# Optimization experiments

Measured on AMD Instinct MI355X. Metric: run time of the kernel, lower is better.

The kernel has to match this reference:

```python
import jax, jax.numpy as jnp
import numpy as np

LOSS_WEIGHT = 1.0
EPS = 1e-12  # numerical floor under the sqrt (module's eps)


def setup_inputs() -> dict:
    key = jax.random.key(0)
    k1, k2 = jax.random.split(key)
    N, P1, P2, D = 16, 4096, 4096, 2
    point_set_1 = jax.random.normal(k1, (N, P1, D), dtype=jnp.float32)
    point_set_2 = jax.random.normal(k2, (N, P2, D), dtype=jnp.float32)
    return {"point_set_1": point_set_1, "point_set_2": point_set_2}


def _chamfer_per_object(x, y):
    # x: [N, P1, 2], y: [N, P2, 2]
    # Pairwise squared L2 via expansion |x|^2 + |y|^2 - 2<x,y> (avoids [N,P1,P2,2] diff tensor)
    x2 = jnp.sum(x * x, axis=-1)                       # [N, P1]
    y2 = jnp.sum(y * y, axis=-1)                       # [N, P2]
    xy = jnp.einsum('npd,nqd->npq', x, y)              # [N, P1, P2]
    C = jnp.sqrt(jnp.clip(x2[:, :, None] + y2[:, None, :] - 2.0 * xy, EPS))  # [N, P1, P2]
    d1 = jnp.min(C, axis=-1).mean(axis=-1)             # min over P2, mean over P1 -> [N]
    d2 = jnp.min(C, axis=-2).mean(axis=-1)             # min over P1, mean over P2 -> [N]
    return 0.5 * (d1 + d2)                             # [N]


def reference(point_set_1, point_set_2):
    # Vectorized form of the per-object Python loop:
    # each object's chamfer (reduction='mean' over a batch of 1 == identity)
    # is masked by (set_2.sum() >= 0), summed, and divided by n_obj.
    cost = _chamfer_per_object(point_set_1, point_set_2)                 # [N]
    m = (jnp.sum(point_set_2, axis=(-1, -2)) >= 0).astype(cost.dtype)    # [N]
    return jnp.mean(cost * m) * LOSS_WEIGHT                              # scalar
```

## Files before the change

kernel.cpp:

```cpp
#include <hip/hip_runtime.h>
#include <math.h>

#define N_OBJ 16
#define P 4096
#define BLOCK 256
#define EPSF 1e-12f

#define G 96
#define GG (G * G)
#define NGRID (2 * N_OBJ)
#define LO (-6.0f)
#define CELL 0.125f
#define INV_CELL 8.0f
#define BPT (GG / BLOCK)
#define QPB (BLOCK / 4)
#define QBLOCKS (2 * N_OBJ * P / QPB)


__device__ __forceinline__ float wave_sum(float s) {
#pragma unroll
    for (int off = 32; off > 0; off >>= 1)
        s += __shfl_xor(s, off, 64);
    return s;
}

__global__ __launch_bounds__(BLOCK) void k_build(const float* __restrict__ s1,
                                                 const float* __restrict__ s2,
                                                 float2* __restrict__ pts,
                                                 unsigned* __restrict__ binStart,
                                                 unsigned* __restrict__ maskws) {
    int gid = blockIdx.x;
    int n = gid >> 1, t = gid & 1;
    int tid = threadIdx.x;
    const float2* src = (const float2*)(t ? s1 : s2) + n * P;

    __shared__ unsigned cnt[GG];
    __shared__ unsigned wtot[BLOCK / 64];
    __shared__ float wq[BLOCK / 64];

    for (int i = tid; i < GG; i += BLOCK) cnt[i] = 0u;
    __syncthreads();

    float2 p[16];
    int b[16];
    float msum = 0.0f;
#pragma unroll
    for (int k = 0; k < 16; k++) {
        float2 v = src[k * BLOCK + tid];
        p[k] = v;
        msum += v.x + v.y;
        int bx = (int)((v.x - LO) * INV_CELL);
        int by = (int)((v.y - LO) * INV_CELL);
        bx = min(max(bx, 0), G - 1);
        by = min(max(by, 0), G - 1);
        b[k] = by * G + bx;
        atomicAdd(&cnt[b[k]], 1u);
    }
    msum = wave_sum(msum);
    if ((tid & 63) == 0) wq[tid >> 6] = msum;
    __syncthreads();
    if (t == 0 && tid == 0) {
        float total = (wq[0] + wq[1]) + (wq[2] + wq[3]);
        maskws[n] = (total >= 0.0f) ? 1u : 0u;
    }

    unsigned run = 0;
    int base = tid * BPT;
    for (int i = 0; i < BPT; i++) {
        unsigned cv = cnt[base + i];
        cnt[base + i] = run;
        run += cv;
    }
    unsigned x = run;
#pragma unroll
    for (int off = 1; off < 64; off <<= 1) {
        unsigned v = __shfl_up(x, off, 64);
        if ((tid & 63) >= off) x += v;
    }
    if ((tid & 63) == 63) wtot[tid >> 6] = x;
    __syncthreads();
    unsigned wpre = 0;
    for (int w2 = 0; w2 < (tid >> 6); w2++) wpre += wtot[w2];
    unsigned offs = wpre + x - run;
    for (int i = 0; i < BPT; i++) cnt[base + i] += offs;
    __syncthreads();

    unsigned* bs = binStart + (size_t)gid * (GG + 1);
    for (int i = tid; i < GG; i += BLOCK) bs[i] = cnt[i];
    if (tid == 0) bs[GG] = P;
    __syncthreads();

    float2* dst = pts + (size_t)gid * P;
#pragma unroll
    for (int k = 0; k < 16; k++) {
        unsigned idx = atomicAdd(&cnt[b[k]], 1u);
        dst[idx] = p[k];
    }
}

#define CAND_LOOP(ss, ee)                                   \
    for (unsigned i = (ss) + sub; i < (ee); i += 4) {       \
        float2 y = tp[i];                                   \
        float y2 = fmaf(y.x, y.x, y.y * y.y);               \
        float d  = fmaf(nqy, y.y, y2);                      \
        d = fmaf(nqx, y.x, d);                              \
        m = fminf(m, d);                                    \
    }

__global__ __launch_bounds__(BLOCK) void k_query(const float2* __restrict__ pts,
                                                 const unsigned* __restrict__ binStart,
                                                 const unsigned* __restrict__ maskws,
                                                 float* __restrict__ out) {
    int bid = blockIdx.x;
    int tid = threadIdx.x;
    int sub = tid & 3;
    int qi  = bid * QPB + (tid >> 2);
    int pass = qi >> 16;
    int n    = (qi >> 12) & 15;
    int qoff = qi & 4095;
    __shared__ float wq[BLOCK / 64];

    if (maskws[n] == 0u) return;

    int g_tgt = n * 2 + pass;
    int g_src = n * 2 + (1 - pass);
    const float2* tp   = pts + (size_t)g_tgt * P;
    const unsigned* bs = binStart + (size_t)g_tgt * (GG + 1);

    float2 q = pts[(size_t)g_src * P + qoff];
    float c   = fmaf(q.x, q.x, q.y * q.y);
    float nqx = -2.0f * q.x, nqy = -2.0f * q.y;
    int bx = min(max((int)((q.x - LO) * INV_CELL), 0), G - 1);
    int by = min(max((int)((q.y - LO) * INV_CELL), 0), G - 1);

    float m = INFINITY;

    for (int dy = 0; dy < G; dy++) {
        if (dy >= 2) {
            float bb = (float)(dy - 1) * CELL;
            if (bb * bb > m + c) break;
        }
        float mc = fmaxf(m + c, 0.0f);
        float sr = sqrtf(mc);
        int w = (sr >= 11.9f) ? G : (int)(sr * INV_CELL) + 2;
        int xs = max(bx - w, 0), xe = min(bx + w, G - 1);

        int yU = by + dy, yD = by - dy;
        unsigned sU = 0u, eU = 0u, sD = 0u, eD = 0u;
        if (yU <= G - 1)          { sU = bs[yU * G + xs]; eU = bs[yU * G + xe + 1]; }
        if (dy > 0 && yD >= 0)    { sD = bs[yD * G + xs]; eD = bs[yD * G + xe + 1]; }
        CAND_LOOP(sU, eU)
        CAND_LOOP(sD, eD)

        m = fminf(m, __shfl_xor(m, 1, 64));
        m = fminf(m, __shfl_xor(m, 2, 64));
    }

    float dq = (sub == 0) ? sqrtf(fmaxf(m + c, EPSF)) : 0.0f;
    dq = wave_sum(dq);
    if ((tid & 63) == 0) wq[tid >> 6] = dq;
    __syncthreads();
    if (tid == 0) {
        float sum = (wq[0] + wq[1]) + (wq[2] + wq[3]);
        atomicAdd(out, sum * (0.5f / (float)P / (float)N_OBJ));
    }
}

extern "C" void kernel_launch(void* const* d_in, const int* in_sizes, int n_in,
                              void* d_out, int out_size, void* d_ws, size_t ws_size,
                              hipStream_t stream) {
    const float* s1 = (const float*)d_in[0];
    const float* s2 = (const float*)d_in[1];
    float* out = (float*)d_out;

    float2* pts        = (float2*)d_ws;
    unsigned* binStart = (unsigned*)(pts + NGRID * P);
    unsigned* maskws   = binStart + NGRID * (GG + 1);

    k_build<<<NGRID, BLOCK, 0, stream>>>(s1, s2, pts, binStart, maskws);
    k_query<<<QBLOCKS, BLOCK, 0, stream>>>(pts, binStart, maskws, out);
}
```

Measured before the change: 86.61 us.

## Assign grid rows to sub-lanes instead of striding points within rows

```diff
diff --git a/kernel.cpp b/kernel.cpp
--- a/kernel.cpp
+++ b/kernel.cpp
@@ -98,15 +98,6 @@
     }
 }
 
-#define CAND_LOOP(ss, ee)                                   \
-    for (unsigned i = (ss) + sub; i < (ee); i += 4) {       \
-        float2 y = tp[i];                                   \
-        float y2 = fmaf(y.x, y.x, y.y * y.y);               \
-        float d  = fmaf(nqy, y.y, y2);                      \
-        d = fmaf(nqx, y.x, d);                              \
-        m = fminf(m, d);                                    \
-    }
-
 __global__ __launch_bounds__(BLOCK) void k_query(const float2* __restrict__ pts,
                                                  const unsigned* __restrict__ binStart,
                                                  const unsigned* __restrict__ maskws,
@@ -135,25 +126,43 @@
 
     float m = INFINITY;
 
-    for (int dy = 0; dy < G; dy++) {
-        if (dy >= 2) {
-            float bb = (float)(dy - 1) * CELL;
-            if (bb * bb > m + c) break;
-        }
+    for (int s = 0; s < 48; s++) {
         float mc = fmaxf(m + c, 0.0f);
         float sr = sqrtf(mc);
         int w = (sr >= 11.9f) ? G : (int)(sr * INV_CELL) + 2;
         int xs = max(bx - w, 0), xe = min(bx + w, G - 1);
 
-        int yU = by + dy, yD = by - dy;
-        unsigned sU = 0u, eU = 0u, sD = 0u, eD = 0u;
-        if (yU <= G - 1)          { sU = bs[yU * G + xs]; eU = bs[yU * G + xe + 1]; }
-        if (dy > 0 && yD >= 0)    { sD = bs[yD * G + xs]; eD = bs[yD * G + xe + 1]; }
-        CAND_LOOP(sU, eU)
-        CAND_LOOP(sD, eD)
+        int k = 4 * s + sub;
+        int off = (k & 1) ? ((k + 1) >> 1) : -(k >> 1);
+        int y = by + off;
+
+        unsigned ss = 0u, ee = 0u;
+        if (0 <= y && y < G) {
+            ss = bs[y * G + xs];
+            ee = bs[y * G + xe + 1];
+        }
+        unsigned i = ss;
+        for (; i + 1 < ee; i += 2) {
+            float2 y0 = tp[i];
+            float2 y1 = tp[i + 1];
+            float a2 = fmaf(y0.x, y0.x, y0.y * y0.y);
+            float b2 = fmaf(y1.x, y1.x, y1.y * y1.y);
+            float da = fmaf(nqx, y0.x, fmaf(nqy, y0.y, a2));
+            float db = fmaf(nqx, y1.x, fmaf(nqy, y1.y, b2));
+            m = fminf(m, fminf(da, db));
+        }
+        if (i < ee) {
+            float2 y0 = tp[i];
+            float a2 = fmaf(y0.x, y0.x, y0.y * y0.y);
+            float da = fmaf(nqx, y0.x, fmaf(nqy, y0.y, a2));
+            m = fminf(m, da);
+        }
 
         m = fminf(m, __shfl_xor(m, 1, 64));
         m = fminf(m, __shfl_xor(m, 2, 64));
+
+        float bb = (float)(2 * s + 1) * CELL;
+        if (bb * bb > m + c) break;
     }
 
     float dq = (sub == 0) ? sqrtf(fmaxf(m + c, EPSF)) : 0.0f;
```

Result: slower. 142.4 us (+64.4%).
